# Performance work log

Measured on AMD Instinct MI355X. Metric: run time of the kernel, lower is better.

## Reference

```python
import jax, jax.numpy as jnp
import numpy as np


def setup_inputs() -> dict:
    key = jax.random.key(0)
    k0, k1, k2, k3, k4, k5 = jax.random.split(key, 6)
    L1, L2, B, D = 512, 512, 32, 1024
    inputs1 = jax.random.normal(k0, (L1, B, D), dtype=jnp.float32)
    inputs2 = jax.random.normal(k1, (L2, B, D), dtype=jnp.float32)
    # mask value 0 marks a valid token (module keeps pairs where both masks == 0)
    mask1 = jax.random.randint(k2, (L1, B), 0, 2, dtype=jnp.int64)
    mask2 = jax.random.randint(k3, (L2, B), 0, 2, dtype=jnp.int64)
    W = jax.random.normal(k4, (D, D), dtype=jnp.float32) * 0.02
    b = jax.random.normal(k5, (1,), dtype=jnp.float32) * 0.02
    return {"inputs1": inputs1, "inputs2": inputs2, "mask1": mask1,
            "mask2": mask2, "W": W, "b": b, "k": 256}


def reference(inputs1, inputs2, mask1, mask2, W, b, k):
    # inputs: [len, bsz, hdim]; masks: [len, bsz]
    H1 = jnp.transpose(inputs1, (1, 0, 2))  # [B, L1, D]
    H2 = jnp.transpose(inputs2, (1, 0, 2))  # [B, L2, D]
    # bilinear scores: H1 @ W @ H2^T + b, then relu  -> [B, L1, L2]
    S = jax.nn.relu(jnp.einsum('bid,de,bje->bij', H1, W, H2) + b[0])
    # pair is valid iff both mask entries are 0
    valid = (mask1.T[:, :, None] == 0) & (mask2.T[:, None, :] == 0)  # [B, L1, L2]
    B = S.shape[0]
    S_flat = jnp.where(valid.reshape(B, -1), S.reshape(B, -1), -jnp.inf)
    num_elems = S_flat.shape[1]
    k_actual = min(k, num_elems)
    q, _ = jax.lax.top_k(S_flat, k_actual)  # [B, k_actual]
    # replace -inf tail entries with the last finite value in each row
    neg = jnp.isneginf(q)
    q_num_finite = k_actual - neg.sum(axis=-1)  # [B]
    fill = jnp.take_along_axis(q, (q_num_finite - 1)[:, None], axis=1)  # [B, 1]
    q = jnp.where(neg, fill, q)
    if k_actual < k:
        q = jnp.concatenate(
            [q, jnp.broadcast_to(q[:, -1:], (B, k - k_actual))], axis=1)
    return q
```

## Files before the change

### kernel.cpp

```cpp
#include <hip/hip_runtime.h>

typedef __bf16 bf16_t;
typedef bf16_t bf16x8 __attribute__((ext_vector_type(8)));
typedef float floatx4 __attribute__((ext_vector_type(4)));

#define L1C 512
#define L2C 512
#define BC  32
#define DC  1024
#define KTOP 256
#define NBIN 4096
#define CAP  1024
#define FBUF 16384

__device__ __forceinline__ unsigned short f2bf(float f) {
    unsigned u = __float_as_uint(f);
    u += 0x7FFFu + ((u >> 16) & 1u);
    return (unsigned short)(u >> 16);
}

__device__ __forceinline__ void g2l16(const unsigned short* g, unsigned short* l) {
    __builtin_amdgcn_global_load_lds((const unsigned int*)g, (unsigned int*)l,
                                     16, 0, 0);
}

__device__ __forceinline__ float decode_key(unsigned k) {
    return __uint_as_float(k & 0x7FFFFFFFu);
}

__global__ void cast_bf16_kernel(const float* __restrict__ src,
                                 unsigned short* __restrict__ dst, int n4) {
    int i = blockIdx.x * blockDim.x + threadIdx.x;
    if (i < n4) {
        float4 v = reinterpret_cast<const float4*>(src)[i];
        ushort4 o;
        o.x = f2bf(v.x); o.y = f2bf(v.y); o.z = f2bf(v.z); o.w = f2bf(v.w);
        reinterpret_cast<ushort4*>(dst)[i] = o;
    }
}

__global__ void transpose_cast_kernel(const float* __restrict__ W,
                                      unsigned short* __restrict__ Wt) {
    __shared__ float tile[32][33];
    int d0 = blockIdx.x * 32, e0 = blockIdx.y * 32;
    int tx = threadIdx.x;
    for (int i = threadIdx.y; i < 32; i += 8)
        tile[i][tx] = W[(size_t)(d0 + i) * DC + e0 + tx];
    __syncthreads();
    for (int i = threadIdx.y; i < 32; i += 8)
        Wt[(size_t)(e0 + i) * DC + d0 + tx] = f2bf(tile[tx][i]);
}

__global__ void init_kernel(unsigned* __restrict__ cnt) {
    int gid = blockIdx.x * blockDim.x + threadIdx.x;
    if (gid < BC * 16) cnt[gid] = 0;
}

__global__ __launch_bounds__(256) void gemm1_kernel(
    const unsigned short* __restrict__ A,
    const unsigned short* __restrict__ Bt,
    unsigned short* __restrict__ C) {
    __shared__ unsigned short As[128][32];
    __shared__ unsigned short Bs[128][32];
    int tid = threadIdx.x;
    int wave = tid >> 6, lane = tid & 63;
    int lane15 = lane & 15, quad = lane >> 4;
    int wm = wave >> 1, wn = wave & 1;
    size_t m0 = (size_t)blockIdx.x * 128, n0 = (size_t)blockIdx.y * 128;

    floatx4 zero = {0.f, 0.f, 0.f, 0.f};
    floatx4 acc[4][4];
#pragma unroll
    for (int i = 0; i < 4; i++)
#pragma unroll
        for (int j = 0; j < 4; j++) acc[i][j] = zero;

    for (int k0 = 0; k0 < DC; k0 += 32) {
#pragma unroll
        for (int c = 0; c < 2; c++) {
            int cid = c * 256 + tid;
            int row = cid >> 2, col8 = (cid & 3) * 8;
            unsigned short* lbase = &As[0][0] + (c * 256 + wave * 64) * 8;
            g2l16(&A[(m0 + row) * DC + k0 + col8], lbase);
            unsigned short* lbase2 = &Bs[0][0] + (c * 256 + wave * 64) * 8;
            g2l16(&Bt[(n0 + row) * DC + k0 + col8], lbase2);
        }
        __syncthreads();
        bf16x8 af[4], bfr[4];
#pragma unroll
        for (int mi = 0; mi < 4; mi++)
            af[mi] = *reinterpret_cast<const bf16x8*>(&As[wm * 64 + mi * 16 + lane15][quad * 8]);
#pragma unroll
        for (int ni = 0; ni < 4; ni++)
            bfr[ni] = *reinterpret_cast<const bf16x8*>(&Bs[wn * 64 + ni * 16 + lane15][quad * 8]);
#pragma unroll
        for (int mi = 0; mi < 4; mi++)
#pragma unroll
            for (int ni = 0; ni < 4; ni++)
                acc[mi][ni] = __builtin_amdgcn_mfma_f32_16x16x32_bf16(
                    af[mi], bfr[ni], acc[mi][ni], 0, 0, 0);
        __syncthreads();
    }
#pragma unroll
    for (int mi = 0; mi < 4; mi++)
#pragma unroll
        for (int ni = 0; ni < 4; ni++)
#pragma unroll
            for (int r = 0; r < 4; r++) {
                size_t row = m0 + wm * 64 + mi * 16 + quad * 4 + r;
                size_t col = n0 + wn * 64 + ni * 16 + lane15;
                C[row * DC + col] = f2bf(acc[mi][ni][r]);
            }
}

__global__ __launch_bounds__(256) void gemm2_kernel(
    const unsigned short* __restrict__ Tm,
    const unsigned short* __restrict__ H2,
    const int* __restrict__ mask1, const int* __restrict__ mask2,
    const float* __restrict__ bptr,
    unsigned* __restrict__ cand,
    unsigned* __restrict__ cnt) {
    __shared__ unsigned short As[128][32];
    __shared__ unsigned short Bs[128][32];
    __shared__ unsigned lh[NBIN];
    __shared__ unsigned csum[256];
    __shared__ int m1s[128], m2s[128];
    __shared__ unsigned tsh, lcnt;
    int tid = threadIdx.x;
    int wave = tid >> 6, lane = tid & 63;
    int lane15 = lane & 15, quad = lane >> 4;
    int wm = wave >> 1, wn = wave & 1;
    int m0 = blockIdx.x * 128, n0 = blockIdx.y * 128;
    int b = blockIdx.z;
    int gblk = b * 16 + blockIdx.y * 4 + blockIdx.x;
    const size_t ldr = (size_t)BC * DC;
    const unsigned short* Ab = Tm + (size_t)b * DC;
    const unsigned short* Bb = H2 + (size_t)b * DC;

    for (int i = tid; i < NBIN; i += 256) lh[i] = 0;
    if (tid < 128) m1s[tid] = (mask1[(m0 + tid) * BC + b] == 0);
    else           m2s[tid - 128] = (mask2[(n0 + tid - 128) * BC + b] == 0);

    floatx4 zero = {0.f, 0.f, 0.f, 0.f};
    floatx4 acc[4][4];
#pragma unroll
    for (int i = 0; i < 4; i++)
#pragma unroll
        for (int j = 0; j < 4; j++) acc[i][j] = zero;

    for (int k0 = 0; k0 < DC; k0 += 32) {
#pragma unroll
        for (int c = 0; c < 2; c++) {
            int cid = c * 256 + tid;
            int row = cid >> 2, col8 = (cid & 3) * 8;
            unsigned short* lbase = &As[0][0] + (c * 256 + wave * 64) * 8;
            g2l16(&Ab[(size_t)(m0 + row) * ldr + k0 + col8], lbase);
            unsigned short* lbase2 = &Bs[0][0] + (c * 256 + wave * 64) * 8;
            g2l16(&Bb[(size_t)(n0 + row) * ldr + k0 + col8], lbase2);
        }
        __syncthreads();
        bf16x8 af[4], bfr[4];
#pragma unroll
        for (int mi = 0; mi < 4; mi++)
            af[mi] = *reinterpret_cast<const bf16x8*>(&As[wm * 64 + mi * 16 + lane15][quad * 8]);
#pragma unroll
        for (int ni = 0; ni < 4; ni++)
            bfr[ni] = *reinterpret_cast<const bf16x8*>(&Bs[wn * 64 + ni * 16 + lane15][quad * 8]);
#pragma unroll
        for (int mi = 0; mi < 4; mi++)
#pragma unroll
            for (int ni = 0; ni < 4; ni++)
                acc[mi][ni] = __builtin_amdgcn_mfma_f32_16x16x32_bf16(
                    af[mi], bfr[ni], acc[mi][ni], 0, 0, 0);
        __syncthreads();
    }

    float bias = bptr[0];
    unsigned zc = 0;
#pragma unroll
    for (int ni = 0; ni < 4; ni++) {
        int jl = wn * 64 + ni * 16 + lane15;
        int v2 = m2s[jl];
#pragma unroll
        for (int mi = 0; mi < 4; mi++)
#pragma unroll
            for (int r = 0; r < 4; r++) {
                int il = wm * 64 + mi * 16 + quad * 4 + r;
                float s = acc[mi][ni][r] + bias;
                if (v2 && m1s[il]) {
                    if (s > 0.f)
                        atomicAdd(&lh[(__float_as_uint(s) | 0x80000000u) >> 20], 1u);
                    else
                        zc++;
                }
            }
    }
    if (zc) atomicAdd(&lh[2048], zc);
    __syncthreads();
    unsigned s16 = 0;
#pragma unroll
    for (int i = 0; i < 16; i++) s16 += lh[tid * 16 + i];
    csum[tid] = s16;
    __syncthreads();
    if (tid == 0) {
        unsigned cum = 0, bin = 2048;
        int found = 0;
        for (int c = 255; c >= 128 && !found; --c) {
            unsigned cs = csum[c];
            if (cum + cs >= KTOP) {
                for (int bb = c * 16 + 15; bb >= c * 16; --bb) {
                    unsigned h = lh[bb];
                    if (cum + h >= KTOP) { bin = (unsigned)bb; found = 1; break; }
                    cum += h;
                }
            } else cum += cs;
        }
        tsh = bin << 20;
        lcnt = 0;
    }
    __syncthreads();
    unsigned T = tsh;
    unsigned base = (unsigned)gblk * CAP;
#pragma unroll
    for (int ni = 0; ni < 4; ni++) {
        int jl = wn * 64 + ni * 16 + lane15;
        int v2 = m2s[jl];
#pragma unroll
        for (int mi = 0; mi < 4; mi++)
#pragma unroll
            for (int r = 0; r < 4; r++) {
                int il = wm * 64 + mi * 16 + quad * 4 + r;
                float s = acc[mi][ni][r] + bias;
                s = s > 0.f ? s : 0.f;
                unsigned key = (v2 && m1s[il])
                                   ? (__float_as_uint(s) | 0x80000000u) : 0u;
                if (key >= T) {
                    unsigned p = atomicAdd(&lcnt, 1u);
                    if (p < CAP) cand[base + p] = key;
                }
            }
    }
    __syncthreads();
    if (tid == 0) cnt[gblk] = lcnt < CAP ? lcnt : CAP;
}

__global__ __launch_bounds__(1024) void final_kernel(
    const unsigned* __restrict__ cand, const unsigned* __restrict__ cnt,
    float* __restrict__ out) {
    __shared__ unsigned buf[FBUF];
    __shared__ unsigned h[NBIN];
    __shared__ unsigned ss[256];
    __shared__ unsigned scnt_s[16], off_s[16];
    __shared__ unsigned ntot_s, sel_c, sel_a, B_s, R_s, mcount;
    __shared__ int have_s;
    __shared__ unsigned srt[256];
    int b = blockIdx.x, tid = threadIdx.x;

    if (tid < 16) {
        unsigned c = cnt[b * 16 + tid];
        scnt_s[tid] = c < CAP ? c : CAP;
    }
    __syncthreads();
    if (tid == 0) {
        unsigned o = 0;
        for (int i = 0; i < 16; i++) { off_s[i] = o; o += scnt_s[i]; }
        ntot_s = o;
        have_s = 1;
    }
    __syncthreads();
    for (int blk = 0; blk < 16; blk++) {
        unsigned c = scnt_s[blk], o = off_s[blk];
        const unsigned* p = cand + (size_t)(b * 16 + blk) * CAP;
        for (unsigned i = tid; i < c; i += 1024) buf[o + i] = p[i];
    }
    __syncthreads();
    unsigned n = ntot_s;

    unsigned Kr = KTOP;
    unsigned pfx = 0;
    unsigned kth = 0;
    for (int pass = 0; pass < 3; pass++) {
        int bins = (pass < 2) ? NBIN : 256;
        int shift = (pass == 0) ? 20 : (pass == 1) ? 8 : 0;
        int nch = bins >> 4;
        for (int i = tid; i < bins; i += 1024) h[i] = 0;
        __syncthreads();
        for (unsigned i = tid; i < n; i += 1024) {
            unsigned k = buf[i];
            bool ok = (pass == 0) ||
                      (pass == 1 && (k >> 20) == pfx) ||
                      (pass == 2 && (k >> 8) == pfx);
            if (ok) atomicAdd(&h[(k >> shift) & (bins - 1)], 1u);
        }
        __syncthreads();
        if (tid < nch) {
            unsigned s = 0;
#pragma unroll
            for (int i = 0; i < 16; i++) s += h[tid * 16 + i];
            ss[tid] = s;
        }
        __syncthreads();
        for (int off = 1; off < nch; off <<= 1) {
            unsigned v = 0;
            if (tid < nch && tid + (unsigned)off < (unsigned)nch) v = ss[tid + off];
            __syncthreads();
            if (tid < nch) ss[tid] += v;
            __syncthreads();
        }
        if (pass == 0) {
            if (tid == 0) have_s = (ss[0] >= KTOP);
            __syncthreads();
            if (!have_s) break;
        }
        if (tid < nch) {
            unsigned above = (tid + 1 < (unsigned)nch) ? ss[tid + 1] : 0u;
            if (above < Kr && ss[tid] >= Kr) { sel_c = tid; sel_a = above; }
        }
        __syncthreads();
        if (tid == 0) {
            unsigned cum = sel_a;
            for (int bb = (int)sel_c * 16 + 15; bb >= (int)sel_c * 16; --bb) {
                unsigned hb = h[bb];
                if (cum + hb >= Kr) { B_s = (unsigned)bb; R_s = Kr - cum; break; }
                cum += hb;
            }
        }
        __syncthreads();
        unsigned Bv = B_s;
        Kr = R_s;
        if (pass == 0) pfx = Bv;
        else if (pass == 1) pfx = (pfx << 12) | Bv;
        else kth = (pfx << 8) | Bv;
        __syncthreads();
    }

    if (tid == 0) mcount = 0;
    __syncthreads();
    int have = have_s;
    unsigned lim = have ? kth : 0u;
    for (unsigned i = tid; i < n; i += 1024) {
        unsigned k = buf[i];
        if (k > lim) {
            unsigned p = atomicAdd(&mcount, 1u);
            if (p < 256) srt[p] = k;
        }
    }
    __syncthreads();
    unsigned m = mcount;
    if (tid < 256 && tid >= (int)m) srt[tid] = have ? kth : 0u;
    for (int k2 = 2; k2 <= 256; k2 <<= 1) {
        for (int j2 = k2 >> 1; j2 > 0; j2 >>= 1) {
            __syncthreads();
            if (tid < 256) {
                int ixj = tid ^ j2;
                if (ixj > tid) {
                    unsigned a = srt[tid], c = srt[ixj];
                    bool up = (tid & k2) == 0;
                    if (up ? (a < c) : (a > c)) { srt[tid] = c; srt[ixj] = a; }
                }
            }
        }
    }
    __syncthreads();
    if (tid < 256) {
        unsigned nval = have ? KTOP : (m < KTOP ? m : KTOP);
        float v;
        if ((unsigned)tid < nval) v = decode_key(srt[tid]);
        else v = (nval > 0) ? decode_key(srt[nval - 1]) : -__builtin_inff();
        out[b * KTOP + tid] = v;
    }
}

extern "C" void kernel_launch(void* const* d_in, const int* in_sizes, int n_in,
                              void* d_out, int out_size, void* d_ws, size_t ws_size,
                              hipStream_t stream) {
    const float* in1   = (const float*)d_in[0];
    const float* in2   = (const float*)d_in[1];
    const int*   mask1 = (const int*)d_in[2];
    const int*   mask2 = (const int*)d_in[3];
    const float* W     = (const float*)d_in[4];
    const float* bias  = (const float*)d_in[5];
    float* out = (float*)d_out;

    char* ws = (char*)d_ws;
    size_t off = 0;
    const size_t nElem = (size_t)L1C * BC * DC;
    unsigned short* A1 = (unsigned short*)(ws + off); off += nElem * 2;
    unsigned short* A2 = (unsigned short*)(ws + off); off += nElem * 2;
    unsigned short* Wt = (unsigned short*)(ws + off); off += (size_t)DC * DC * 2;
    unsigned short* Tm = (unsigned short*)(ws + off); off += nElem * 2;
    unsigned* cand = (unsigned*)(ws + off); off += (size_t)BC * 16 * CAP * 4;
    unsigned* cnt  = (unsigned*)(ws + off); off += (size_t)BC * 16 * 4;

    int n4 = (int)(nElem / 4);
    cast_bf16_kernel<<<n4 / 256, 256, 0, stream>>>(in1, A1, n4);
    cast_bf16_kernel<<<n4 / 256, 256, 0, stream>>>(in2, A2, n4);
    transpose_cast_kernel<<<dim3(DC / 32, DC / 32), dim3(32, 8), 0, stream>>>(W, Wt);
    init_kernel<<<2, 256, 0, stream>>>(cnt);

    gemm1_kernel<<<dim3(128, 8), 256, 0, stream>>>(A1, Wt, Tm);
    gemm2_kernel<<<dim3(4, 4, BC), 256, 0, stream>>>(Tm, A2, mask1, mask2, bias,
                                                     cand, cnt);
    final_kernel<<<BC, 1024, 0, stream>>>(cand, cnt, out);
}
```

Before: 292.2 us.

## Transpose inputs to batch-major during bf16 cast and remap gemm2 blocks per XCD

The fp32-to-bf16 cast now also reorders inputs from [L,B,D] to [B,L,D], so gemm2 reads contiguous rows with stride D instead of B*D. Masks are likewise pre-transposed into batch-major buffers in the init kernel. gemm2 becomes a 1D grid whose block index is decoded so that all tiles of a batch land on the same XCD, aiming for better L2 reuse of Tm and H2. Tm is written by gemm1 from the reordered A1, so it inherits the batch-major layout. The cast kernel now launches one block per row, which is a much larger grid and may add launch overhead.

New measurement: 281.1 us. -3.8%, faster.

```diff
diff --git a/kernel.cpp b/kernel.cpp
--- a/kernel.cpp
+++ b/kernel.cpp
@@ -28,15 +28,27 @@
     return __uint_as_float(k & 0x7FFFFFFFu);
 }
 
-__global__ void cast_bf16_kernel(const float* __restrict__ src,
-                                 unsigned short* __restrict__ dst, int n4) {
-    int i = blockIdx.x * blockDim.x + threadIdx.x;
-    if (i < n4) {
-        float4 v = reinterpret_cast<const float4*>(src)[i];
-        ushort4 o;
-        o.x = f2bf(v.x); o.y = f2bf(v.y); o.z = f2bf(v.z); o.w = f2bf(v.w);
-        reinterpret_cast<ushort4*>(dst)[i] = o;
-    }
+__global__ __launch_bounds__(256) void cast_tr_kernel(
+    const float* __restrict__ in1, const float* __restrict__ in2,
+    unsigned short* __restrict__ A1, unsigned short* __restrict__ A2) {
+    int r = blockIdx.x;
+    const float* src;
+    unsigned short* dst;
+    if (r < L1C * BC) {
+        int l = r >> 5, b = r & 31;
+        src = in1 + (size_t)r * DC;
+        dst = A1 + ((size_t)b * L1C + l) * DC;
+    } else {
+        int r2 = r - L1C * BC;
+        int l = r2 >> 5, b = r2 & 31;
+        src = in2 + (size_t)r2 * DC;
+        dst = A2 + ((size_t)b * L2C + l) * DC;
+    }
+    int t = threadIdx.x;
+    float4 v = reinterpret_cast<const float4*>(src)[t];
+    ushort4 o;
+    o.x = f2bf(v.x); o.y = f2bf(v.y); o.z = f2bf(v.z); o.w = f2bf(v.w);
+    reinterpret_cast<ushort4*>(dst)[t] = o;
 }
 
 __global__ void transpose_cast_kernel(const float* __restrict__ W,
@@ -51,8 +63,16 @@
         Wt[(size_t)(e0 + i) * DC + d0 + tx] = f2bf(tile[tx][i]);
 }
 
-__global__ void init_kernel(unsigned* __restrict__ cnt) {
+__global__ void init_kernel(const int* __restrict__ mask1,
+                            const int* __restrict__ mask2,
+                            int* __restrict__ m1t, int* __restrict__ m2t,
+                            unsigned* __restrict__ cnt) {
     int gid = blockIdx.x * blockDim.x + threadIdx.x;
+    if (gid < L1C * BC) {
+        int l = gid & 511, b = gid >> 9;
+        m1t[gid] = mask1[(l << 5) + b];
+        m2t[gid] = mask2[(l << 5) + b];
+    }
     if (gid < BC * 16) cnt[gid] = 0;
 }
 
@@ -116,7 +136,7 @@
 __global__ __launch_bounds__(256) void gemm2_kernel(
     const unsigned short* __restrict__ Tm,
     const unsigned short* __restrict__ H2,
-    const int* __restrict__ mask1, const int* __restrict__ mask2,
+    const int* __restrict__ m1t, const int* __restrict__ m2t,
     const float* __restrict__ bptr,
     unsigned* __restrict__ cand,
     unsigned* __restrict__ cnt) {
@@ -130,16 +150,18 @@
     int wave = tid >> 6, lane = tid & 63;
     int lane15 = lane & 15, quad = lane >> 4;
     int wm = wave >> 1, wn = wave & 1;
-    int m0 = blockIdx.x * 128, n0 = blockIdx.y * 128;
-    int b = blockIdx.z;
-    int gblk = b * 16 + blockIdx.y * 4 + blockIdx.x;
-    const size_t ldr = (size_t)BC * DC;
-    const unsigned short* Ab = Tm + (size_t)b * DC;
-    const unsigned short* Bb = H2 + (size_t)b * DC;
+    int L = blockIdx.x;
+    int xcd = L & 7, tile = (L >> 3) & 15, chunk = L >> 7;
+    int b = xcd + (chunk << 3);
+    int bx = tile & 3, by = tile >> 2;
+    int m0 = bx * 128, n0 = by * 128;
+    int gblk = b * 16 + by * 4 + bx;
+    const unsigned short* Ab = Tm + (size_t)b * L1C * DC;
+    const unsigned short* Bb = H2 + (size_t)b * L2C * DC;
 
     for (int i = tid; i < NBIN; i += 256) lh[i] = 0;
-    if (tid < 128) m1s[tid] = (mask1[(m0 + tid) * BC + b] == 0);
-    else           m2s[tid - 128] = (mask2[(n0 + tid - 128) * BC + b] == 0);
+    if (tid < 128) m1s[tid] = (m1t[b * L1C + m0 + tid] == 0);
+    else           m2s[tid - 128] = (m2t[b * L2C + n0 + tid - 128] == 0);
 
     floatx4 zero = {0.f, 0.f, 0.f, 0.f};
     floatx4 acc[4][4];
@@ -154,9 +176,9 @@
             int cid = c * 256 + tid;
             int row = cid >> 2, col8 = (cid & 3) * 8;
             unsigned short* lbase = &As[0][0] + (c * 256 + wave * 64) * 8;
-            g2l16(&Ab[(size_t)(m0 + row) * ldr + k0 + col8], lbase);
+            g2l16(&Ab[(size_t)(m0 + row) * DC + k0 + col8], lbase);
             unsigned short* lbase2 = &Bs[0][0] + (c * 256 + wave * 64) * 8;
-            g2l16(&Bb[(size_t)(n0 + row) * ldr + k0 + col8], lbase2);
+            g2l16(&Bb[(size_t)(n0 + row) * DC + k0 + col8], lbase2);
         }
         __syncthreads();
         bf16x8 af[4], bfr[4];
@@ -391,15 +413,14 @@
     unsigned short* Tm = (unsigned short*)(ws + off); off += nElem * 2;
     unsigned* cand = (unsigned*)(ws + off); off += (size_t)BC * 16 * CAP * 4;
     unsigned* cnt  = (unsigned*)(ws + off); off += (size_t)BC * 16 * 4;
-
-    int n4 = (int)(nElem / 4);
-    cast_bf16_kernel<<<n4 / 256, 256, 0, stream>>>(in1, A1, n4);
-    cast_bf16_kernel<<<n4 / 256, 256, 0, stream>>>(in2, A2, n4);
+    int* m1t = (int*)(ws + off); off += (size_t)BC * L1C * 4;
+    int* m2t = (int*)(ws + off); off += (size_t)BC * L2C * 4;
+
+    cast_tr_kernel<<<2 * L1C * BC, 256, 0, stream>>>(in1, in2, A1, A2);
     transpose_cast_kernel<<<dim3(DC / 32, DC / 32), dim3(32, 8), 0, stream>>>(W, Wt);
-    init_kernel<<<2, 256, 0, stream>>>(cnt);
+    init_kernel<<<64, 256, 0, stream>>>(mask1, mask2, m1t, m2t, cnt);
 
     gemm1_kernel<<<dim3(128, 8), 256, 0, stream>>>(A1, Wt, Tm);
-    gemm2_kernel<<<dim3(4, 4, BC), 256, 0, stream>>>(Tm, A2, mask1, mask2, bias,
-                                                     cand, cnt);
+    gemm2_kernel<<<512, 256, 0, stream>>>(Tm, A2, m1t, m2t, bias, cand, cnt);
     final_kernel<<<BC, 1024, 0, stream>>>(cand, cnt, out);
 }
```
